# Optimization experiments

Hardware: AMD Instinct MI355X
Metric: run time of the kernel (lower is better)

## Reference

```python
import jax, jax.numpy as jnp
import numpy as np

DEPTH = 16      # env_depth: number of sequential beam-search steps
TEMP = 20.0     # softmax temperature (forward default temp=20)
NEG = -1e9      # -inf surrogate for dead beams (grad-safe)


def setup_inputs() -> dict:
    key = jax.random.key(0)
    ks = jax.random.split(key, 7)
    B, H, D = 256, 512, 64
    u = lambda k, s: jax.random.uniform(k, s, jnp.float32, -0.1, 0.1)
    return {
        "env": jax.random.normal(ks[0], (B, D), jnp.float32),
        "root_state": u(ks[1], (1, H)),
        "W_logits": u(ks[2], (H, D)),
        "b_logits": u(ks[3], (D,)),
        "W_hh": u(ks[4], (H, H)),
        "b_hh": u(ks[5], (H,)),
        "emb": u(ks[6], (D, H)),
        "beams": 128,
    }


def reference(env, root_state, W_logits, b_logits, W_hh, b_hh, emb, beams):
    B = env.shape[0]
    H = root_state.shape[1]
    D = W_logits.shape[1]

    # All beams start at the (shared, learned) root state; only beam 0 is live.
    states = jnp.broadcast_to(root_state[None, :, :], (B, beams, H))  # [B, K, H]
    scores = jnp.where(jnp.arange(beams) == 0, 0.0, NEG).astype(jnp.float32)
    scores = jnp.broadcast_to(scores[None, :], (B, beams))            # [B, K]
    hist = jnp.zeros((B, beams, DEPTH), jnp.int32)                    # chosen decisions

    def step(carry, t):
        states, scores, hist = carry
        # RNN router step: logits over decisions, temperature-scaled log-softmax
        logits = jnp.einsum('bkh,hd->bkd', states, W_logits) + b_logits  # [B,K,D]
        logp = jax.nn.log_softmax(logits / TEMP, axis=-1)
        # cumulative beam scores over all beams*decisions candidates
        cand = (scores[..., None] + logp).reshape(B, beams * D)
        top_scores, top_idx = jax.lax.top_k(cand, beams)                 # [B,K]
        beam_idx = top_idx // D                                          # parent beam
        dec = top_idx % D                                                # chosen decision
        # gather surviving beam state + history
        sel = jnp.take_along_axis(states, beam_idx[..., None], axis=1)   # [B,K,H]
        hist = jnp.take_along_axis(hist, beam_idx[..., None], axis=1)
        hist = hist.at[:, :, t].set(dec)
        # recurrent state update conditioned on chosen decision
        new_states = jnp.tanh(jnp.einsum('bkh,hg->bkg', sel, W_hh) + b_hh + emb[dec])
        return (new_states, top_scores, hist), None

    (states, scores, hist), _ = jax.lax.scan(step, (states, scores, hist), jnp.arange(DEPTH))
    return hist, scores
```

## Files before the change

### kernel.cpp

```cpp
#include <hip/hip_runtime.h>
#include <hip/hip_bf16.h>
#include <math.h>

#define NB    256
#define NK    128
#define NH    512
#define ND    64
#define NDEPTH 16
#define BKROWS (NB*NK)
#define TEMPD 20.0

typedef double d4 __attribute__((ext_vector_type(4)));

__global__ void k_prep(const float* __restrict__ Whh, const float* __restrict__ Wl,
                       double* __restrict__ Wsw, double* __restrict__ Wld) {
    int idx = blockIdx.x * 256 + threadIdx.x;
    int k = idx >> 9;
    int c = idx & 511;
    int cb = c >> 7, cl = c & 127;
    Wsw[((size_t)cb * NH + k) * 128 + cl] = (double)Whh[idx];
    if (idx < NH * ND) Wld[idx] = (double)Wl[idx];
}

__global__ void k_init(const float* __restrict__ root, float* __restrict__ states,
                       double* __restrict__ scores, unsigned char* __restrict__ hist) {
    int idx = blockIdx.x * 256 + threadIdx.x;
    states[idx] = root[idx & (NH - 1)];
    if (idx < BKROWS) scores[idx] = ((idx & (NK - 1)) == 0) ? 0.0 : -1e9;
    if (idx < BKROWS * NDEPTH) hist[idx] = 0;
}

__global__ void __launch_bounds__(256, 4)
k_logits(const float* __restrict__ states,
         const double* __restrict__ Wld,
         const float* __restrict__ bl,
         const double* __restrict__ scores,
         double* __restrict__ cand)
{
    __shared__ double wl[16][64];
    __shared__ double st[64][16];
    const int rowb = blockIdx.x * 64;
    const int t    = threadIdx.x;
    const int tc   = t & 31;
    const int rg   = t >> 5;

    double acc[8][2];
    #pragma unroll
    for (int i = 0; i < 8; ++i) { acc[i][0] = 0.0; acc[i][1] = 0.0; }

    for (int kc = 0; kc < NH; kc += 16) {
        #pragma unroll
        for (int j = 0; j < 2; ++j) {
            int idx = j * 256 + t;
            int row = idx >> 5, cp = idx & 31;
            double2 d = *(const double2*)&Wld[(size_t)(kc + row) * ND + 2 * cp];
            *(double2*)&wl[row][2 * cp] = d;
        }
        #pragma unroll
        for (int j = 0; j < 2; ++j) {
            int idx = j * 256 + t;
            int r = idx >> 3, cp = idx & 7;
            float2 v = *(const float2*)&states[(size_t)(rowb + r) * NH + kc + 2 * cp];
            double2 d; d.x = (double)v.x; d.y = (double)v.y;
            *(double2*)&st[r][2 * cp] = d;
        }
        __syncthreads();
        #pragma unroll 4
        for (int hh = 0; hh < 16; hh += 2) {
            double w00 = wl[hh][tc],   w01 = wl[hh][tc+32];
            double w10 = wl[hh+1][tc], w11 = wl[hh+1][tc+32];
            #pragma unroll
            for (int i = 0; i < 8; ++i) {
                double2 s = *(const double2*)&st[rg*8+i][hh];
                acc[i][0] = fma(s.x, w00, acc[i][0]);
                acc[i][1] = fma(s.x, w01, acc[i][1]);
                acc[i][0] = fma(s.y, w10, acc[i][0]);
                acc[i][1] = fma(s.y, w11, acc[i][1]);
            }
        }
        __syncthreads();
    }

    const double bd0 = (double)bl[tc];
    const double bd1 = (double)bl[tc + 32];
    #pragma unroll
    for (int i = 0; i < 8; ++i) {
        int row = rowb + rg * 8 + i;
        double x0 = (acc[i][0] + bd0) / TEMPD;
        double x1 = (acc[i][1] + bd1) / TEMPD;
        double m = fmax(x0, x1);
        for (int off = 1; off <= 16; off <<= 1) m = fmax(m, __shfl_xor(m, off, 64));
        double e = exp(x0 - m) + exp(x1 - m);
        for (int off = 1; off <= 16; off <<= 1) e += __shfl_xor(e, off, 64);
        double ls = log(e);
        double sc = scores[row];
        cand[(size_t)row * ND + tc]      = sc + x0 - m - ls;
        cand[(size_t)row * ND + tc + 32] = sc + x1 - m - ls;
    }
}

__global__ void __launch_bounds__(256)
k_topk(const double* __restrict__ cand,
       double* __restrict__ scores,
       int* __restrict__ parent, int* __restrict__ decs,
       const unsigned char* __restrict__ hist_in,
       unsigned char* __restrict__ hist_out,
       int tstep)
{
    extern __shared__ double smem[];
    double* L  = smem;
    int*    sp = (int*)(smem + 128 * 65);
    int*    sd = sp + NK;

    const int b = blockIdx.x;
    const int t = threadIdx.x;
    const double* cb = cand + (size_t)b * (NK * ND);

    #pragma unroll
    for (int j = 0; j < 32; ++j) {
        int i = j * 256 + t;
        L[(i >> 6) * 65 + (i & 63)] = cb[i];
    }
    __syncthreads();

    if (t < 64) {
        const int lane = t;
        double mv = L[lane]; int mi = lane;
        for (int i = 1; i < 128; ++i) {
            double v = L[i * 65 + lane];
            if (v > mv) { mv = v; mi = i * 64 + lane; }
        }
        for (int it = 0; it < NK; ++it) {
            double m = mv; int idx = mi;
            #pragma unroll
            for (int off = 1; off <= 32; off <<= 1) {
                double m2 = __shfl_xor(m, off, 64);
                int    i2 = __shfl_xor(idx, off, 64);
                if (m2 > m || (m2 == m && i2 < idx)) { m = m2; idx = i2; }
            }
            const int wrow = idx >> 6, wcol = idx & 63;
            if (lane == 0) {
                scores[b * NK + it] = m;
                parent[b * NK + it] = wrow;
                decs  [b * NK + it] = wcol;
                sp[it] = wrow; sd[it] = wcol;
            }
            if (lane == wcol) L[wrow * 65 + wcol] = -INFINITY;
            double r0 = L[(2 * lane) * 65 + wcol];
            double r1 = L[(2 * lane + 1) * 65 + wcol];
            double rm; int ri;
            if (r1 > r0) { rm = r1; ri = (2 * lane + 1) * 64 + wcol; }
            else         { rm = r0; ri = (2 * lane) * 64 + wcol; }
            #pragma unroll
            for (int off = 1; off <= 32; off <<= 1) {
                double m2 = __shfl_xor(rm, off, 64);
                int    i2 = __shfl_xor(ri, off, 64);
                if (m2 > rm || (m2 == rm && i2 < ri)) { rm = m2; ri = i2; }
            }
            if (lane == wcol) { mv = rm; mi = ri; }
        }
    }
    __syncthreads();

    for (int i = t; i < NK * NDEPTH; i += 256) {
        int k = i >> 4, j = i & 15;
        hist_out[(b * NK + k) * NDEPTH + j] = (j == tstep) ? (unsigned char)sd[k]
                                            : hist_in[(b * NK + sp[k]) * NDEPTH + j];
    }
}

__global__ void __launch_bounds__(256, 4)
k_rnn(const float* __restrict__ states_in,
      const double* __restrict__ Wsw,
      const float* __restrict__ bhh,
      const float* __restrict__ emb,
      const int* __restrict__ parent, const int* __restrict__ decs,
      float* __restrict__ states_out)
{
    __shared__ double wt[16][128];
    __shared__ double st[64][18];
    __shared__ int sp[64], sd[64];

    const int rowb = blockIdx.x * 64;
    const int cbk  = blockIdx.y;
    const int colb = cbk * 128;
    const int t    = threadIdx.x;
    const int lane = t & 63;
    const int wv   = t >> 6;
    const int li   = lane & 15;
    const int kq   = lane >> 4;
    const int wm   = wv >> 1;
    const int wn   = wv & 1;

    if (t < 64) { sp[t] = parent[rowb + t]; sd[t] = decs[rowb + t]; }
    __syncthreads();

    int srow[2];
    #pragma unroll
    for (int j = 0; j < 2; ++j) {
        int r = (j * 256 + t) >> 3;
        srow[j] = ((rowb + r) >> 7) * NK + sp[r];
    }

    d4 acc[2][4];
    #pragma unroll
    for (int i = 0; i < 2; ++i)
        #pragma unroll
        for (int j = 0; j < 4; ++j) { acc[i][j][0]=0.0; acc[i][j][1]=0.0; acc[i][j][2]=0.0; acc[i][j][3]=0.0; }

    const double* wsb = Wsw + (size_t)cbk * NH * 128;

    for (int kc = 0; kc < NH; kc += 16) {
        #pragma unroll
        for (int j = 0; j < 4; ++j) {
            int idx = j * 256 + t;
            int row = idx >> 6, cp = idx & 63;
            double2 d = *(const double2*)&wsb[(size_t)(kc + row) * 128 + 2 * cp];
            *(double2*)&wt[row][2 * cp] = d;
        }
        #pragma unroll
        for (int j = 0; j < 2; ++j) {
            int idx = j * 256 + t;
            int r = idx >> 3, cp = idx & 7;
            float2 v = *(const float2*)&states_in[(size_t)srow[j] * NH + kc + 2 * cp];
            double2 d; d.x = (double)v.x; d.y = (double)v.y;
            *(double2*)&st[r][2 * cp] = d;
        }
        __syncthreads();

        #pragma unroll
        for (int ks = 0; ks < 4; ++ks) {
            const int kk = ks * 4 + kq;
            double a0 = st[wm * 32 + li][kk];
            double a1 = st[wm * 32 + 16 + li][kk];
            const double* wrow = &wt[kk][wn * 64];
            double b0 = wrow[li];
            double b1 = wrow[16 + li];
            double b2 = wrow[32 + li];
            double b3 = wrow[48 + li];
            acc[0][0] = __builtin_amdgcn_mfma_f64_16x16x4f64(a0, b0, acc[0][0], 0, 0, 0);
            acc[0][1] = __builtin_amdgcn_mfma_f64_16x16x4f64(a0, b1, acc[0][1], 0, 0, 0);
            acc[0][2] = __builtin_amdgcn_mfma_f64_16x16x4f64(a0, b2, acc[0][2], 0, 0, 0);
            acc[0][3] = __builtin_amdgcn_mfma_f64_16x16x4f64(a0, b3, acc[0][3], 0, 0, 0);
            acc[1][0] = __builtin_amdgcn_mfma_f64_16x16x4f64(a1, b0, acc[1][0], 0, 0, 0);
            acc[1][1] = __builtin_amdgcn_mfma_f64_16x16x4f64(a1, b1, acc[1][1], 0, 0, 0);
            acc[1][2] = __builtin_amdgcn_mfma_f64_16x16x4f64(a1, b2, acc[1][2], 0, 0, 0);
            acc[1][3] = __builtin_amdgcn_mfma_f64_16x16x4f64(a1, b3, acc[1][3], 0, 0, 0);
        }
        __syncthreads();
    }

    #pragma unroll
    for (int ct = 0; ct < 4; ++ct) {
        int col = colb + wn * 64 + ct * 16 + li;
        double bb = (double)bhh[col];
        #pragma unroll
        for (int rt = 0; rt < 2; ++rt) {
            #pragma unroll
            for (int n = 0; n < 4; ++n) {
                int rL = wm * 32 + rt * 16 + kq + 4 * n;
                double e = (double)emb[(size_t)sd[rL] * NH + col];
                double z = acc[rt][ct][n] + bb + e;
                states_out[(size_t)(rowb + rL) * NH + col] = (float)tanh(z);
            }
        }
    }
}

__global__ void k_final(const unsigned char* __restrict__ hist,
                        const double* __restrict__ scores,
                        float* __restrict__ out)
{
    int i = blockIdx.x * 256 + threadIdx.x;
    const int nh = BKROWS * NDEPTH;
    if (i < nh) out[i] = (float)hist[i];
    else if (i < nh + BKROWS) out[i] = (float)scores[i - nh];
}

extern "C" void kernel_launch(void* const* d_in, const int* in_sizes, int n_in,
                              void* d_out, int out_size, void* d_ws, size_t ws_size,
                              hipStream_t stream) {
    const float* root = (const float*)d_in[1];
    const float* Wl   = (const float*)d_in[2];
    const float* bl   = (const float*)d_in[3];
    const float* Whh  = (const float*)d_in[4];
    const float* bhh  = (const float*)d_in[5];
    const float* emb  = (const float*)d_in[6];

    char* ws = (char*)d_ws;
    double* Wsw          = (double*)(ws + 0);
    double* Wld          = (double*)(ws + 2097152);
    double* cand         = (double*)(ws + 2359296);
    double* scores       = (double*)(ws + 19136512);
    float*  sA           = (float*)(ws + 19398656);
    float*  sB           = (float*)(ws + 86507520);
    int*    parent       = (int*)(ws + 153616384);
    int*    decs         = (int*)(ws + 153747456);
    unsigned char* hA    = (unsigned char*)(ws + 153878528);
    unsigned char* hB    = (unsigned char*)(ws + 154402816);

    k_prep<<<1024, 256, 0, stream>>>(Whh, Wl, Wsw, Wld);
    k_init<<<65536, 256, 0, stream>>>(root, sA, scores, hA);

    float* scur = sA; float* snxt = sB;
    unsigned char* hcur = hA; unsigned char* hnxt = hB;
    for (int t = 0; t < NDEPTH; ++t) {
        k_logits<<<512, 256, 0, stream>>>(scur, Wld, bl, scores, cand);
        k_topk<<<256, 256, 67584, stream>>>(cand, scores, parent, decs, hcur, hnxt, t);
        k_rnn<<<dim3(512, 4), 256, 0, stream>>>(scur, Wsw, bhh, emb, parent, decs, snxt);
        { float* tmp = scur; scur = snxt; snxt = tmp; }
        { unsigned char* tmp = hcur; hcur = hnxt; hnxt = tmp; }
    }

    k_final<<<2176, 256, 0, stream>>>(hcur, scores, (float*)d_out);
}
```

Baseline: 8.862 ms.

## Move logits GEMM to FP64 MFMA and stream transposed weights via direct-to-LDS loads

```diff
diff --git a/kernel.cpp b/kernel.cpp
--- a/kernel.cpp
+++ b/kernel.cpp
@@ -12,14 +12,19 @@
 
 typedef double d4 __attribute__((ext_vector_type(4)));
 
+__device__ __forceinline__ void load_lds16(const void* g, void* l) {
+    __builtin_amdgcn_global_load_lds(
+        (const __attribute__((address_space(1))) unsigned int*)g,
+        (__attribute__((address_space(3))) unsigned int*)l, 16, 0, 0);
+}
+
 __global__ void k_prep(const float* __restrict__ Whh, const float* __restrict__ Wl,
-                       double* __restrict__ Wsw, double* __restrict__ Wld) {
+                       double* __restrict__ WswT, double* __restrict__ WldT) {
     int idx = blockIdx.x * 256 + threadIdx.x;
-    int k = idx >> 9;
-    int c = idx & 511;
-    int cb = c >> 7, cl = c & 127;
-    Wsw[((size_t)cb * NH + k) * 128 + cl] = (double)Whh[idx];
-    if (idx < NH * ND) Wld[idx] = (double)Wl[idx];
+    int k = idx & 511;
+    int c = idx >> 9;
+    WswT[(size_t)c * NH + k] = (double)Whh[(size_t)k * NH + c];
+    if (c < ND) WldT[(size_t)c * NH + k] = (double)Wl[(size_t)k * ND + c];
 }
 
 __global__ void k_init(const float* __restrict__ root, float* __restrict__ states,
@@ -32,70 +37,86 @@
 
 __global__ void __launch_bounds__(256, 4)
 k_logits(const float* __restrict__ states,
-         const double* __restrict__ Wld,
+         const double* __restrict__ WldT,
          const float* __restrict__ bl,
          const double* __restrict__ scores,
          double* __restrict__ cand)
 {
-    __shared__ double wl[16][64];
-    __shared__ double st[64][16];
+    __shared__ double wlT[64][18];
+    __shared__ double stT[16][66];
     const int rowb = blockIdx.x * 64;
     const int t    = threadIdx.x;
-    const int tc   = t & 31;
-    const int rg   = t >> 5;
-
-    double acc[8][2];
-    #pragma unroll
-    for (int i = 0; i < 8; ++i) { acc[i][0] = 0.0; acc[i][1] = 0.0; }
+    const int lane = t & 63;
+    const int wv   = t >> 6;
+    const int li   = lane & 15;
+    const int kq   = lane >> 4;
+
+    d4 acc[4];
+    #pragma unroll
+    for (int c = 0; c < 4; ++c) { acc[c][0]=0.0; acc[c][1]=0.0; acc[c][2]=0.0; acc[c][3]=0.0; }
+
+    const char* wbase = (const char*)WldT;
 
     for (int kc = 0; kc < NH; kc += 16) {
         #pragma unroll
-        for (int j = 0; j < 2; ++j) {
-            int idx = j * 256 + t;
-            int row = idx >> 5, cp = idx & 31;
-            double2 d = *(const double2*)&Wld[(size_t)(kc + row) * ND + 2 * cp];
-            *(double2*)&wl[row][2 * cp] = d;
+        for (int i = 0; i < 3; ++i) {
+            int n = wv + 4 * i;
+            if (n < 9) {
+                int c = n * 64 + lane;
+                int col = c / 9, j9 = c - col * 9;
+                load_lds16(wbase + (size_t)col * 4096 + j9 * 16 + kc * 8,
+                           (char*)&wlT[0][0] + n * 1024);
+            }
         }
         #pragma unroll
         for (int j = 0; j < 2; ++j) {
             int idx = j * 256 + t;
             int r = idx >> 3, cp = idx & 7;
             float2 v = *(const float2*)&states[(size_t)(rowb + r) * NH + kc + 2 * cp];
-            double2 d; d.x = (double)v.x; d.y = (double)v.y;
-            *(double2*)&st[r][2 * cp] = d;
+            stT[2 * cp][r]     = (double)v.x;
+            stT[2 * cp + 1][r] = (double)v.y;
         }
         __syncthreads();
-        #pragma unroll 4
-        for (int hh = 0; hh < 16; hh += 2) {
-            double w00 = wl[hh][tc],   w01 = wl[hh][tc+32];
-            double w10 = wl[hh+1][tc], w11 = wl[hh+1][tc+32];
-            #pragma unroll
-            for (int i = 0; i < 8; ++i) {
-                double2 s = *(const double2*)&st[rg*8+i][hh];
-                acc[i][0] = fma(s.x, w00, acc[i][0]);
-                acc[i][1] = fma(s.x, w01, acc[i][1]);
-                acc[i][0] = fma(s.y, w10, acc[i][0]);
-                acc[i][1] = fma(s.y, w11, acc[i][1]);
-            }
+
+        #pragma unroll
+        for (int ks = 0; ks < 4; ++ks) {
+            int kk = 4 * ks + kq;
+            double a  = stT[kk][wv * 16 + li];
+            double b0 = wlT[     li][kk];
+            double b1 = wlT[16 + li][kk];
+            double b2 = wlT[32 + li][kk];
+            double b3 = wlT[48 + li][kk];
+            acc[0] = __builtin_amdgcn_mfma_f64_16x16x4f64(a, b0, acc[0], 0, 0, 0);
+            acc[1] = __builtin_amdgcn_mfma_f64_16x16x4f64(a, b1, acc[1], 0, 0, 0);
+            acc[2] = __builtin_amdgcn_mfma_f64_16x16x4f64(a, b2, acc[2], 0, 0, 0);
+            acc[3] = __builtin_amdgcn_mfma_f64_16x16x4f64(a, b3, acc[3], 0, 0, 0);
         }
         __syncthreads();
     }
 
-    const double bd0 = (double)bl[tc];
-    const double bd1 = (double)bl[tc + 32];
-    #pragma unroll
-    for (int i = 0; i < 8; ++i) {
-        int row = rowb + rg * 8 + i;
-        double x0 = (acc[i][0] + bd0) / TEMPD;
-        double x1 = (acc[i][1] + bd1) / TEMPD;
-        double m = fmax(x0, x1);
-        for (int off = 1; off <= 16; off <<= 1) m = fmax(m, __shfl_xor(m, off, 64));
-        double e = exp(x0 - m) + exp(x1 - m);
-        for (int off = 1; off <= 16; off <<= 1) e += __shfl_xor(e, off, 64);
+    const double bd0 = (double)bl[li];
+    const double bd1 = (double)bl[16 + li];
+    const double bd2 = (double)bl[32 + li];
+    const double bd3 = (double)bl[48 + li];
+    #pragma unroll
+    for (int n = 0; n < 4; ++n) {
+        int row = rowb + wv * 16 + kq + 4 * n;
+        double x0 = (acc[0][n] + bd0) / TEMPD;
+        double x1 = (acc[1][n] + bd1) / TEMPD;
+        double x2 = (acc[2][n] + bd2) / TEMPD;
+        double x3 = (acc[3][n] + bd3) / TEMPD;
+        double m = fmax(fmax(x0, x1), fmax(x2, x3));
+        #pragma unroll
+        for (int off = 1; off <= 8; off <<= 1) m = fmax(m, __shfl_xor(m, off, 64));
+        double e = exp(x0 - m) + exp(x1 - m) + exp(x2 - m) + exp(x3 - m);
+        #pragma unroll
+        for (int off = 1; off <= 8; off <<= 1) e += __shfl_xor(e, off, 64);
         double ls = log(e);
         double sc = scores[row];
-        cand[(size_t)row * ND + tc]      = sc + x0 - m - ls;
-        cand[(size_t)row * ND + tc + 32] = sc + x1 - m - ls;
+        cand[(size_t)row * ND +      li] = sc + x0 - m - ls;
+        cand[(size_t)row * ND + 16 + li] = sc + x1 - m - ls;
+        cand[(size_t)row * ND + 32 + li] = sc + x2 - m - ls;
+        cand[(size_t)row * ND + 48 + li] = sc + x3 - m - ls;
     }
 }
 
@@ -171,14 +192,14 @@
 
 __global__ void __launch_bounds__(256, 4)
 k_rnn(const float* __restrict__ states_in,
-      const double* __restrict__ Wsw,
+      const double* __restrict__ WswT,
       const float* __restrict__ bhh,
       const float* __restrict__ emb,
       const int* __restrict__ parent, const int* __restrict__ decs,
       float* __restrict__ states_out)
 {
-    __shared__ double wt[16][128];
-    __shared__ double st[64][18];
+    __shared__ double wtT[128][18];
+    __shared__ double stT[16][66];
     __shared__ int sp[64], sd[64];
 
     const int rowb = blockIdx.x * 64;
@@ -208,36 +229,38 @@
         #pragma unroll
         for (int j = 0; j < 4; ++j) { acc[i][j][0]=0.0; acc[i][j][1]=0.0; acc[i][j][2]=0.0; acc[i][j][3]=0.0; }
 
-    const double* wsb = Wsw + (size_t)cbk * NH * 128;
+    const char* wbase = (const char*)(WswT + (size_t)colb * NH);
 
     for (int kc = 0; kc < NH; kc += 16) {
         #pragma unroll
-        for (int j = 0; j < 4; ++j) {
-            int idx = j * 256 + t;
-            int row = idx >> 6, cp = idx & 63;
-            double2 d = *(const double2*)&wsb[(size_t)(kc + row) * 128 + 2 * cp];
-            *(double2*)&wt[row][2 * cp] = d;
+        for (int i = 0; i < 5; ++i) {
+            int n = wv + 4 * i;
+            if (n < 18) {
+                int c = n * 64 + lane;
+                int col = c / 9, j9 = c - col * 9;
+                load_lds16(wbase + (size_t)col * 4096 + j9 * 16 + kc * 8,
+                           (char*)&wtT[0][0] + n * 1024);
+            }
         }
         #pragma unroll
         for (int j = 0; j < 2; ++j) {
             int idx = j * 256 + t;
             int r = idx >> 3, cp = idx & 7;
             float2 v = *(const float2*)&states_in[(size_t)srow[j] * NH + kc + 2 * cp];
-            double2 d; d.x = (double)v.x; d.y = (double)v.y;
-            *(double2*)&st[r][2 * cp] = d;
+            stT[2 * cp][r]     = (double)v.x;
+            stT[2 * cp + 1][r] = (double)v.y;
         }
         __syncthreads();
 
         #pragma unroll
         for (int ks = 0; ks < 4; ++ks) {
-            const int kk = ks * 4 + kq;
-            double a0 = st[wm * 32 + li][kk];
-            double a1 = st[wm * 32 + 16 + li][kk];
-            const double* wrow = &wt[kk][wn * 64];
-            double b0 = wrow[li];
-            double b1 = wrow[16 + li];
-            double b2 = wrow[32 + li];
-            double b3 = wrow[48 + li];
+            int kk = 4 * ks + kq;
+            double a0 = stT[kk][wm * 32 + li];
+            double a1 = stT[kk][wm * 32 + 16 + li];
+            double b0 = wtT[wn * 64 +      li][kk];
+            double b1 = wtT[wn * 64 + 16 + li][kk];
+            double b2 = wtT[wn * 64 + 32 + li][kk];
+            double b3 = wtT[wn * 64 + 48 + li][kk];
             acc[0][0] = __builtin_amdgcn_mfma_f64_16x16x4f64(a0, b0, acc[0][0], 0, 0, 0);
             acc[0][1] = __builtin_amdgcn_mfma_f64_16x16x4f64(a0, b1, acc[0][1], 0, 0, 0);
             acc[0][2] = __builtin_amdgcn_mfma_f64_16x16x4f64(a0, b2, acc[0][2], 0, 0, 0);
@@ -288,26 +311,26 @@
     const float* emb  = (const float*)d_in[6];
 
     char* ws = (char*)d_ws;
-    double* Wsw          = (double*)(ws + 0);
-    double* Wld          = (double*)(ws + 2097152);
-    double* cand         = (double*)(ws + 2359296);
-    double* scores       = (double*)(ws + 19136512);
-    float*  sA           = (float*)(ws + 19398656);
-    float*  sB           = (float*)(ws + 86507520);
-    int*    parent       = (int*)(ws + 153616384);
-    int*    decs         = (int*)(ws + 153747456);
-    unsigned char* hA    = (unsigned char*)(ws + 153878528);
-    unsigned char* hB    = (unsigned char*)(ws + 154402816);
-
-    k_prep<<<1024, 256, 0, stream>>>(Whh, Wl, Wsw, Wld);
+    double* WswT         = (double*)(ws + 0);
+    double* WldT         = (double*)(ws + 2097408);
+    double* cand         = (double*)(ws + 2359808);
+    double* scores       = (double*)(ws + 19137024);
+    float*  sA           = (float*)(ws + 19399168);
+    float*  sB           = (float*)(ws + 86508032);
+    int*    parent       = (int*)(ws + 153616896);
+    int*    decs         = (int*)(ws + 153747968);
+    unsigned char* hA    = (unsigned char*)(ws + 153879040);
+    unsigned char* hB    = (unsigned char*)(ws + 154403328);
+
+    k_prep<<<1024, 256, 0, stream>>>(Whh, Wl, WswT, WldT);
     k_init<<<65536, 256, 0, stream>>>(root, sA, scores, hA);
 
     float* scur = sA; float* snxt = sB;
     unsigned char* hcur = hA; unsigned char* hnxt = hB;
     for (int t = 0; t < NDEPTH; ++t) {
-        k_logits<<<512, 256, 0, stream>>>(scur, Wld, bl, scores, cand);
+        k_logits<<<512, 256, 0, stream>>>(scur, WldT, bl, scores, cand);
         k_topk<<<256, 256, 67584, stream>>>(cand, scores, parent, decs, hcur, hnxt, t);
-        k_rnn<<<dim3(512, 4), 256, 0, stream>>>(scur, Wsw, bhh, emb, parent, decs, snxt);
+        k_rnn<<<dim3(512, 4), 256, 0, stream>>>(scur, WswT, bhh, emb, parent, decs, snxt);
         { float* tmp = scur; scur = snxt; snxt = tmp; }
         { unsigned char* tmp = hcur; hcur = hnxt; hnxt = tmp; }
     }
```

New measurement: 8.797 ms. Within noise of the previous version (-0.7%).
